# Kernel optimization log

Hardware: AMD Instinct MI355X
Metric: run time of the kernel (lower is better)

## Reference

```python
import jax, jax.numpy as jnp
import numpy as np

N_HEADS = 12
NEG_BIG = 1e10  # matches torch source's -10000000000.0 masking constant


def setup_inputs() -> dict:
    key = jax.random.key(0)
    ks = jax.random.split(key, 5)
    nb, ns, nf = 4, 2048, 768
    return {
        "x": jax.random.normal(ks[0], (nb, ns, nf), dtype=jnp.float32),
        "Wqkv_w": jax.random.normal(ks[1], (3 * nf, nf), dtype=jnp.float32) * 0.02,
        "Wqkv_b": jax.random.normal(ks[2], (3 * nf,), dtype=jnp.float32) * 0.02,
        "Wproj_w": jax.random.normal(ks[3], (nf, nf), dtype=jnp.float32) * 0.02,
        "Wproj_b": jax.random.normal(ks[4], (nf,), dtype=jnp.float32) * 0.02,
    }


def reference(x, Wqkv_w, Wqkv_b, Wproj_w, Wproj_b):
    nb, ns, nf = x.shape
    hd = nf // N_HEADS
    qkv = x @ Wqkv_w.T + Wqkv_b            # [b, s, 3f]
    q = qkv[..., :nf]                       # source bug: k and v are taken from q
    q = q.reshape(nb, ns, N_HEADS, hd).transpose(0, 2, 1, 3)  # [b, h, s, d]
    k = q
    v = q
    w = jnp.einsum("bhqd,bhkd->bhqk", q, k) * (1.0 / jnp.sqrt(jnp.float32(hd)))
    mask = jnp.tril(jnp.ones((ns, ns), dtype=x.dtype))
    w = jax.nn.softmax(w * mask - NEG_BIG * (1.0 - mask), axis=-1)
    a = jnp.einsum("bhqk,bhkd->bhqd", w, v)
    a = a.transpose(0, 2, 1, 3).reshape(nb, ns, nf)
    return a @ Wproj_w.T + Wproj_b
```

## Files before the change

### kernel.cpp

```cpp
#include <hip/hip_runtime.h>
#include <hip/hip_bf16.h>

#define NF 768
#define NHEADS 12
#define NSEQ 2048
#define NX (8192 * 768)
#define NW (768 * 768)

#define QSC 0.42466090f

typedef __attribute__((__ext_vector_type__(8))) __bf16 bfrag;
typedef __attribute__((__ext_vector_type__(4))) float f32x4;
typedef __attribute__((__ext_vector_type__(16))) float f32x16;

static __device__ __forceinline__ unsigned short bfu(float f) {
    union { __hip_bfloat16 h; unsigned short u; } v;
    v.h = __float2bfloat16(f);
    return v.u;
}

static __device__ __forceinline__ int packrn(float lo, float hi) {
    union { __hip_bfloat162 h; int i; } u;
    u.h.x = __float2bfloat16(lo);
    u.h.y = __float2bfloat16(hi);
    return u.i;
}

static __device__ __forceinline__ float exp2a(float x) {
#if __has_builtin(__builtin_amdgcn_exp2f)
    return __builtin_amdgcn_exp2f(x);
#else
    return exp2f(x);
#endif
}

static __device__ __forceinline__ void plswap(int& a, int& b, int hi) {
#if __has_builtin(__builtin_amdgcn_permlane32_swap)
    auto r = __builtin_amdgcn_permlane32_swap((unsigned)a, (unsigned)b, false, false);
    a = (int)r[0]; b = (int)r[1];
#else
    int ta = __shfl_xor(b, 32), tb = __shfl_xor(a, 32);
    a = hi ? ta : a;
    b = hi ? b : tb;
#endif
}

static __device__ __forceinline__ float xhalf(float v, int hi) {
#if __has_builtin(__builtin_amdgcn_permlane32_swap)
    union { float f; unsigned u; } c; c.f = v;
    auto r = __builtin_amdgcn_permlane32_swap(c.u, c.u, false, false);
    union { unsigned u; float f; } d; d.u = hi ? r[0] : r[1];
    return d.f;
#else
    return __shfl_xor(v, 32);
#endif
}

static __device__ __forceinline__ void gload16(const unsigned short* g, unsigned short* l) {
#if __has_builtin(__builtin_amdgcn_global_load_lds)
    __builtin_amdgcn_global_load_lds(
        (const __attribute__((address_space(1))) void*)g,
        (__attribute__((address_space(3))) void*)l, 16, 0, 0);
#else
    *(uint4*)l = *(const uint4*)g;
#endif
}

__global__ __launch_bounds__(256) void preconv(const float* __restrict__ x,
                                               const float* __restrict__ W1,
                                               const float* __restrict__ W2,
                                               unsigned short* __restrict__ xb,
                                               unsigned short* __restrict__ W1b,
                                               unsigned short* __restrict__ W2b) {
    const size_t i = ((size_t)blockIdx.x * 256 + threadIdx.x) * 8;
    const float* src;
    unsigned short* dst;
    float scl = 1.0f;
    if (i < (size_t)NX) {
        src = x + i; dst = xb + i;
    } else if (i < (size_t)NX + NW) {
        const size_t j = i - NX;
        src = W1 + j; dst = W1b + j; scl = QSC;
    } else {
        const size_t j = i - NX - NW;
        src = W2 + j; dst = W2b + j;
    }
    float4 v0 = *(const float4*)(src);
    float4 v1 = *(const float4*)(src + 4);
    uint4 o;
    o.x = (unsigned)packrn(v0.x * scl, v0.y * scl);
    o.y = (unsigned)packrn(v0.z * scl, v0.w * scl);
    o.z = (unsigned)packrn(v1.x * scl, v1.y * scl);
    o.w = (unsigned)packrn(v1.z * scl, v1.w * scl);
    *(uint4*)dst = o;
}

__global__ __launch_bounds__(256) void gemm_qkv(const unsigned short* __restrict__ A,
                                                const unsigned short* __restrict__ B,
                                                const float* __restrict__ bias,
                                                unsigned short* __restrict__ Qo) {
    __shared__ unsigned short As[64 * 32];
    __shared__ unsigned short Bs[128 * 32];
    const int t    = threadIdx.x;
    const int bm   = blockIdx.x / 6, bn = blockIdx.x % 6;
    const int m0   = bm * 64, n0 = bn * 128;
    const int lane = t & 63;
    const int wid  = t >> 6;
    const int wm   = (wid >> 1) * 32, wn = (wid & 1) * 64;

    const unsigned short* ga  = A + (size_t)(m0 + (t >> 2)) * NF + (t & 3) * 8;
    const unsigned short* gb  = B + (size_t)(n0 + (t >> 2)) * NF + (t & 3) * 8;
    const unsigned short* gb2 = gb + (size_t)64 * NF;

    f32x4 acc[2][4];
#pragma unroll
    for (int i = 0; i < 2; i++)
#pragma unroll
        for (int j = 0; j < 4; j++) acc[i][j] = (f32x4)0.0f;

    for (int k0 = 0; k0 < NF; k0 += 32) {
        gload16(ga + k0, &As[t * 8]);
        gload16(gb + k0, &Bs[t * 8]);
        gload16(gb2 + k0, &Bs[2048 + t * 8]);
        __syncthreads();

        bfrag af[2], bfr[4];
#pragma unroll
        for (int i = 0; i < 2; i++)
            af[i]  = *(const bfrag*)&As[(wm + i*16 + (lane & 15)) * 32 + (lane >> 4) * 8];
#pragma unroll
        for (int j = 0; j < 4; j++)
            bfr[j] = *(const bfrag*)&Bs[(wn + j*16 + (lane & 15)) * 32 + (lane >> 4) * 8];
#pragma unroll
        for (int i = 0; i < 2; i++)
#pragma unroll
            for (int j = 0; j < 4; j++)
                acc[i][j] = __builtin_amdgcn_mfma_f32_16x16x32_bf16(af[i], bfr[j], acc[i][j], 0, 0, 0);
        __syncthreads();
    }

#pragma unroll
    for (int j = 0; j < 4; j++) {
        const int col = n0 + wn + j*16 + (lane & 15);
        const float bq = QSC * bias[col];
#pragma unroll
        for (int i = 0; i < 2; i++) {
            const int rbase = m0 + wm + i*16 + ((lane >> 4) << 2);
#pragma unroll
            for (int r = 0; r < 4; r++)
                Qo[(size_t)(rbase + r) * NF + col] = bfu(acc[i][j][r] + bq);
        }
    }
}

__global__ __launch_bounds__(256) void gemm_proj(const unsigned short* __restrict__ A,
                                                 const unsigned short* __restrict__ B,
                                                 const float* __restrict__ bias,
                                                 float* __restrict__ out) {
    __shared__ unsigned short As[64 * 32];
    __shared__ unsigned short Bs[128 * 32];
    const int t    = threadIdx.x;
    const int bm   = blockIdx.x / 6, bn = blockIdx.x % 6;
    const int m0   = bm * 64, n0 = bn * 128;
    const int lane = t & 63;
    const int wid  = t >> 6;
    const int wm   = (wid >> 1) * 32, wn = (wid & 1) * 64;

    const unsigned short* ga  = A + (size_t)(m0 + (t >> 2)) * NF + (t & 3) * 8;
    const unsigned short* gb  = B + (size_t)(n0 + (t >> 2)) * NF + (t & 3) * 8;
    const unsigned short* gb2 = gb + (size_t)64 * NF;

    f32x4 acc[2][4];
#pragma unroll
    for (int i = 0; i < 2; i++)
#pragma unroll
        for (int j = 0; j < 4; j++) acc[i][j] = (f32x4)0.0f;

    for (int k0 = 0; k0 < NF; k0 += 32) {
        gload16(ga + k0, &As[t * 8]);
        gload16(gb + k0, &Bs[t * 8]);
        gload16(gb2 + k0, &Bs[2048 + t * 8]);
        __syncthreads();

        bfrag af[2], bfr[4];
#pragma unroll
        for (int i = 0; i < 2; i++)
            af[i]  = *(const bfrag*)&As[(wm + i*16 + (lane & 15)) * 32 + (lane >> 4) * 8];
#pragma unroll
        for (int j = 0; j < 4; j++)
            bfr[j] = *(const bfrag*)&Bs[(wn + j*16 + (lane & 15)) * 32 + (lane >> 4) * 8];
#pragma unroll
        for (int i = 0; i < 2; i++)
#pragma unroll
            for (int j = 0; j < 4; j++)
                acc[i][j] = __builtin_amdgcn_mfma_f32_16x16x32_bf16(af[i], bfr[j], acc[i][j], 0, 0, 0);
        __syncthreads();
    }

#pragma unroll
    for (int j = 0; j < 4; j++) {
        const int col = n0 + wn + j*16 + (lane & 15);
        const float bvv = bias[col];
#pragma unroll
        for (int i = 0; i < 2; i++) {
            const int rbase = m0 + wm + i*16 + ((lane >> 4) << 2);
#pragma unroll
            for (int r = 0; r < 4; r++)
                out[(size_t)(rbase + r) * NF + col] = acc[i][j][r] + bvv;
        }
    }
}

__global__ __launch_bounds__(128, 1) void attn(const unsigned short* __restrict__ Q,
                                               unsigned short* __restrict__ O) {
    const int pair = blockIdx.x;
    const int bh   = blockIdx.y;
    const int b    = bh / NHEADS, h = bh % NHEADS;
    const unsigned short* base = Q + (size_t)b * NSEQ * NF + h * 64;
    unsigned short*       ob   = O + (size_t)b * NSEQ * NF + h * 64;

    const int t   = threadIdx.x;
    const int w   = t >> 6;
    const int l31 = t & 31;
    const int hi  = (t >> 5) & 1;
    const int sw  = l31 & 7;
    const int svw = (l31 & 7) ^ ((l31 >> 2) & 7);

    __shared__ unsigned short Ks[64 * 64];
    __shared__ unsigned short Vt[64 * 64];

    for (int half = 0; half < 2; half++) {
        const int qt  = half ? (31 - pair) : pair;
        const int wq0 = qt * 64 + w * 32;
        const int qg  = wq0 + l31;

        bfrag qf[4];
#pragma unroll
        for (int c16 = 0; c16 < 4; c16++)
            qf[c16] = *(const bfrag*)(base + (size_t)qg * NF + c16*16 + hi*8);

        f32x16 o[2];
#pragma unroll
        for (int fd = 0; fd < 2; fd++)
#pragma unroll
            for (int r = 0; r < 16; r++) o[fd][r] = 0.0f;
        float m_ = -3.0e38f, l_ = 0.0f;

        const int ktend = qt + 1;
        for (int kt = 0; kt < ktend; kt++) {
            const int k0 = kt * 64;

            {
                const int r = t >> 1, c = t & 1;
                const unsigned short* kg = base + (size_t)(k0 + r) * NF + c * 32;
#pragma unroll
                for (int i = 0; i < 4; i++) {
                    uint4 v = *(const uint4*)(kg + i * 8);
                    const int u = (4 * c + i) ^ (r & 7);
                    *(uint4*)&Ks[r * 64 + u * 8] = v;
                }
            }
            {
                const int p = t & 15, g2 = t >> 4;
                const unsigned short* vg = base + (size_t)(k0 + 8 * g2) * NF + 4 * p;
                uint2 ld[8];
#pragma unroll
                for (int i = 0; i < 8; i++) ld[i] = *(const uint2*)(vg + (size_t)i * NF);
#pragma unroll
                for (int j = 0; j < 4; j++) {
                    const int d = 4 * p + j;
                    union { unsigned short h[8]; uint4 q; } wv;
#pragma unroll
                    for (int i = 0; i < 8; i++) wv.h[i] = ((const unsigned short*)&ld[i])[j];
                    const int u = g2 ^ (d & 7) ^ ((d >> 2) & 7);
                    *(uint4*)&Vt[d * 64 + u * 8] = wv.q;
                }
            }
            __syncthreads();

            const bool diag  = (kt == qt);
            const int  kb_hi = diag ? w : 1;

            f32x16 s[2];
            __builtin_amdgcn_s_setprio(1);
#pragma unroll
            for (int kblk = 0; kblk < 2; kblk++) {
                if (kblk <= kb_hi) {
                    f32x16 z;
#pragma unroll
                    for (int r = 0; r < 16; r++) z[r] = 0.0f;
#pragma unroll
                    for (int c16 = 0; c16 < 4; c16++) {
                        bfrag ka = *(const bfrag*)&Ks[(kblk*32 + l31)*64 + (((2*c16 + hi) ^ sw) * 8)];
                        z = __builtin_amdgcn_mfma_f32_32x32x16_bf16(ka, qf[c16], z, 0, 0, 0);
                    }
                    s[kblk] = z;
                }
            }
            __builtin_amdgcn_s_setprio(0);

            if (diag) {
                if (w == 0) {
#pragma unroll
                    for (int r = 0; r < 16; r++) {
                        const int kp = k0 + (r & 3) + 8*(r >> 2) + 4*hi;
                        if (kp > qg) s[0][r] = -1.0e30f;
                    }
                } else {
#pragma unroll
                    for (int r = 0; r < 16; r++) {
                        const int kp = k0 + 32 + (r & 3) + 8*(r >> 2) + 4*hi;
                        if (kp > qg) s[1][r] = -1.0e30f;
                    }
                }
            }

            float mx = -3.0e38f;
#pragma unroll
            for (int kblk = 0; kblk < 2; kblk++)
                if (kblk <= kb_hi) {
#pragma unroll
                    for (int r = 0; r < 16; r++) mx = fmaxf(mx, s[kblk][r]);
                }
            mx = fmaxf(mx, xhalf(mx, hi));

            const bool nogrow = __all(mx <= m_ + 8.0f);
            const float mn = nogrow ? m_ : fmaxf(m_, mx);
            float rs = 0.0f;
#pragma unroll
            for (int kblk = 0; kblk < 2; kblk++)
                if (kblk <= kb_hi) {
#pragma unroll
                    for (int r = 0; r < 16; r++) {
                        const float p = exp2a(s[kblk][r] - mn);
                        s[kblk][r] = p;
                        rs += p;
                    }
                }
            rs += xhalf(rs, hi);
            if (nogrow) {
                l_ += rs;
            } else {
                const float sc = exp2a(m_ - mn);
                l_ = l_ * sc + rs;
                m_ = mn;
#pragma unroll
                for (int fd = 0; fd < 2; fd++)
#pragma unroll
                    for (int r = 0; r < 16; r++) o[fd][r] *= sc;
            }

#pragma unroll
            for (int kblk = 0; kblk < 2; kblk++) {
                if (kblk <= kb_hi) {
                    int wv_[4][2];
#pragma unroll
                    for (int f = 0; f < 4; f++)
#pragma unroll
                        for (int rr = 0; rr < 2; rr++)
                            wv_[f][rr] = packrn(s[kblk][4*f + 2*rr], s[kblk][4*f + 2*rr + 1]);
#pragma unroll
                    for (int c = 0; c < 2; c++) {
                        int x0 = wv_[2*c][0], y0 = wv_[2*c+1][0];
                        plswap(x0, y0, hi);
                        int x1 = wv_[2*c][1], y1 = wv_[2*c+1][1];
                        plswap(x1, y1, hi);
                        union { int d[4]; bfrag f; } pf;
                        pf.d[0] = x0; pf.d[1] = x1; pf.d[2] = y0; pf.d[3] = y1;
                        const int ck = kblk*2 + c;
                        __builtin_amdgcn_s_setprio(1);
#pragma unroll
                        for (int fd = 0; fd < 2; fd++) {
                            bfrag va = *(const bfrag*)&Vt[(fd*32 + l31)*64 + (((2*ck + hi) ^ svw) * 8)];
                            o[fd] = __builtin_amdgcn_mfma_f32_32x32x16_bf16(va, pf.f, o[fd], 0, 0, 0);
                        }
                        __builtin_amdgcn_s_setprio(0);
                    }
                }
            }
            __syncthreads();
        }

        const float inv = 1.0f / (l_ * QSC);
#pragma unroll
        for (int fd = 0; fd < 2; fd++)
#pragma unroll
            for (int f = 0; f < 4; f++) {
                const int d0 = fd*32 + 8*f + 4*hi;
                uint2 pr;
                pr.x = (unsigned)packrn(o[fd][4*f+0]*inv, o[fd][4*f+1]*inv);
                pr.y = (unsigned)packrn(o[fd][4*f+2]*inv, o[fd][4*f+3]*inv);
                *(uint2*)(ob + (size_t)qg * NF + d0) = pr;
            }
    }
}

extern "C" void kernel_launch(void* const* d_in, const int* in_sizes, int n_in,
                              void* d_out, int out_size, void* d_ws, size_t ws_size,
                              hipStream_t stream) {
    const float* x    = (const float*)d_in[0];
    const float* Wqkv = (const float*)d_in[1];
    const float* bqkv = (const float*)d_in[2];
    const float* Wp   = (const float*)d_in[3];
    const float* bp   = (const float*)d_in[4];
    float* out        = (float*)d_out;

    unsigned short* Qws = (unsigned short*)d_ws;
    unsigned short* Aws = Qws + (size_t)NX;
    unsigned short* xb  = Aws + (size_t)NX;
    unsigned short* W1b = xb + (size_t)NX;
    unsigned short* W2b = W1b + (size_t)NW;

    preconv<<<3648, 256, 0, stream>>>(x, Wqkv, Wp, xb, W1b, W2b);
    gemm_qkv<<<768, 256, 0, stream>>>(xb, W1b, bqkv, Qws);
    attn<<<dim3(16, 48), 128, 0, stream>>>(Qws, Aws);
    gemm_proj<<<768, 256, 0, stream>>>(Aws, W2b, bp, out);
}
```

Before: 131.6 us.

## Double-buffer K/V tiles in attention with register prefetch of next tile

The attention kernel now keeps two LDS buffers for K and transposed V. It issues global loads for the next key tile into registers during the softmax and PV phase, then writes them to the alternate buffer before the barrier, leaving one sync per iteration. The aim is to hide global load latency behind MFMA work. In exchange it doubles LDS use and raises register pressure from the held prefetch values.

```diff
diff --git a/kernel.cpp b/kernel.cpp
--- a/kernel.cpp
+++ b/kernel.cpp
@@ -64,6 +64,34 @@
 #else
     *(uint4*)l = *(const uint4*)g;
 #endif
+}
+
+static __device__ __forceinline__ void loadt(const unsigned short* kgb, const unsigned short* vgb,
+                                             size_t off, uint4 (&kv)[4], uint2 (&vd)[8]) {
+#pragma unroll
+    for (int i = 0; i < 4; i++) kv[i] = *(const uint4*)(kgb + off + i * 8);
+#pragma unroll
+    for (int i = 0; i < 8; i++) vd[i] = *(const uint2*)(vgb + off + (size_t)i * NF);
+}
+
+static __device__ __forceinline__ void writet(int t, const uint4 (&kv)[4], const uint2 (&vd)[8],
+                                              unsigned short* Ksb, unsigned short* Vtb) {
+    const int kr = t >> 1, kc = t & 1;
+#pragma unroll
+    for (int i = 0; i < 4; i++) {
+        const int u = (4 * kc + i) ^ (kr & 7);
+        *(uint4*)&Ksb[kr * 64 + u * 8] = kv[i];
+    }
+    const int vp = t & 15, vg2 = t >> 4;
+#pragma unroll
+    for (int j = 0; j < 4; j++) {
+        const int d = 4 * vp + j;
+        union { unsigned short h[8]; uint4 q; } wv;
+#pragma unroll
+        for (int i = 0; i < 8; i++) wv.h[i] = ((const unsigned short*)&vd[i])[j];
+        const int u = vg2 ^ (d & 7) ^ ((d >> 2) & 7);
+        *(uint4*)&Vtb[d * 64 + u * 8] = wv.q;
+    }
 }
 
 __global__ __launch_bounds__(256) void preconv(const float* __restrict__ x,
@@ -226,8 +254,11 @@
     const int sw  = l31 & 7;
     const int svw = (l31 & 7) ^ ((l31 >> 2) & 7);
 
-    __shared__ unsigned short Ks[64 * 64];
-    __shared__ unsigned short Vt[64 * 64];
+    const unsigned short* kgb = base + (size_t)(t >> 1) * NF + (t & 1) * 32;
+    const unsigned short* vgb = base + (size_t)(8 * (t >> 4)) * NF + 4 * (t & 15);
+
+    __shared__ unsigned short Ks[2][64 * 64];
+    __shared__ unsigned short Vt[2][64 * 64];
 
     for (int half = 0; half < 2; half++) {
         const int qt  = half ? (31 - pair) : pair;
@@ -247,39 +278,20 @@
         float m_ = -3.0e38f, l_ = 0.0f;
 
         const int ktend = qt + 1;
+
+        uint4 kv[4];
+        uint2 vd[8];
+        loadt(kgb, vgb, 0, kv, vd);
+        writet(t, kv, vd, &Ks[0][0], &Vt[0][0]);
+        __syncthreads();
+
         for (int kt = 0; kt < ktend; kt++) {
+            const unsigned short* ksb = &Ks[kt & 1][0];
+            const unsigned short* vtb = &Vt[kt & 1][0];
             const int k0 = kt * 64;
-
-            {
-                const int r = t >> 1, c = t & 1;
-                const unsigned short* kg = base + (size_t)(k0 + r) * NF + c * 32;
-#pragma unroll
-                for (int i = 0; i < 4; i++) {
-                    uint4 v = *(const uint4*)(kg + i * 8);
-                    const int u = (4 * c + i) ^ (r & 7);
-                    *(uint4*)&Ks[r * 64 + u * 8] = v;
-                }
-            }
-            {
-                const int p = t & 15, g2 = t >> 4;
-                const unsigned short* vg = base + (size_t)(k0 + 8 * g2) * NF + 4 * p;
-                uint2 ld[8];
-#pragma unroll
-                for (int i = 0; i < 8; i++) ld[i] = *(const uint2*)(vg + (size_t)i * NF);
-#pragma unroll
-                for (int j = 0; j < 4; j++) {
-                    const int d = 4 * p + j;
-                    union { unsigned short h[8]; uint4 q; } wv;
-#pragma unroll
-                    for (int i = 0; i < 8; i++) wv.h[i] = ((const unsigned short*)&ld[i])[j];
-                    const int u = g2 ^ (d & 7) ^ ((d >> 2) & 7);
-                    *(uint4*)&Vt[d * 64 + u * 8] = wv.q;
-                }
-            }
-            __syncthreads();
-
             const bool diag  = (kt == qt);
             const int  kb_hi = diag ? w : 1;
+            const bool more  = (kt + 1 < ktend);
 
             f32x16 s[2];
             __builtin_amdgcn_s_setprio(1);
@@ -291,7 +303,7 @@
                     for (int r = 0; r < 16; r++) z[r] = 0.0f;
 #pragma unroll
                     for (int c16 = 0; c16 < 4; c16++) {
-                        bfrag ka = *(const bfrag*)&Ks[(kblk*32 + l31)*64 + (((2*c16 + hi) ^ sw) * 8)];
+                        bfrag ka = *(const bfrag*)&ksb[(kblk*32 + l31)*64 + (((2*c16 + hi) ^ sw) * 8)];
                         z = __builtin_amdgcn_mfma_f32_32x32x16_bf16(ka, qf[c16], z, 0, 0, 0);
                     }
                     s[kblk] = z;
@@ -350,6 +362,8 @@
                     for (int r = 0; r < 16; r++) o[fd][r] *= sc;
             }
 
+            if (more) loadt(kgb, vgb, (size_t)(kt + 1) * 64 * NF, kv, vd);
+
 #pragma unroll
             for (int kblk = 0; kblk < 2; kblk++) {
                 if (kblk <= kb_hi) {
@@ -371,13 +385,15 @@
                         __builtin_amdgcn_s_setprio(1);
 #pragma unroll
                         for (int fd = 0; fd < 2; fd++) {
-                            bfrag va = *(const bfrag*)&Vt[(fd*32 + l31)*64 + (((2*ck + hi) ^ svw) * 8)];
+                            bfrag va = *(const bfrag*)&vtb[(fd*32 + l31)*64 + (((2*ck + hi) ^ svw) * 8)];
                             o[fd] = __builtin_amdgcn_mfma_f32_32x32x16_bf16(va, pf.f, o[fd], 0, 0, 0);
                         }
                         __builtin_amdgcn_s_setprio(0);
                     }
                 }
             }
+
+            if (more) writet(t, kv, vd, &Ks[(kt + 1) & 1][0], &Vt[(kt + 1) & 1][0]);
             __syncthreads();
         }
 
```

Measured after the change: 190.8 us. 45.0% more time.

## Use 128-query tiles with 4 waves per attention block, drop pair balancing

Applied to the files above, without the earlier changes.

Each attention block now has 256 threads (4 waves) covering a 128-row query tile, replacing the two-wave block that handled a balanced pair of 64-row tiles in sequence. Blocks are issued longest-first (qt = 15 - blockIdx.x) so the causal imbalance is left to the hardware scheduler instead of the explicit pairing. K tile loading and V transpose loading now run on separate thread halves, and waves whose queries lie entirely before a key tile skip its compute. This shares each K/V tile across more waves, but blocks are now uneven in length, and some waves sit idle on tiles near the diagonal.

```diff
diff --git a/kernel.cpp b/kernel.cpp
--- a/kernel.cpp
+++ b/kernel.cpp
@@ -211,11 +211,11 @@
     }
 }
 
-__global__ __launch_bounds__(128, 1) void attn(const unsigned short* __restrict__ Q,
+__global__ __launch_bounds__(256, 1) void attn(const unsigned short* __restrict__ Q,
                                                unsigned short* __restrict__ O) {
-    const int pair = blockIdx.x;
-    const int bh   = blockIdx.y;
-    const int b    = bh / NHEADS, h = bh % NHEADS;
+    const int qt = 15 - blockIdx.x;
+    const int bh = blockIdx.y;
+    const int b  = bh / NHEADS, h = bh % NHEADS;
     const unsigned short* base = Q + (size_t)b * NSEQ * NF + h * 64;
     unsigned short*       ob   = O + (size_t)b * NSEQ * NF + h * 64;
 
@@ -229,57 +229,56 @@
     __shared__ unsigned short Ks[64 * 64];
     __shared__ unsigned short Vt[64 * 64];
 
-    for (int half = 0; half < 2; half++) {
-        const int qt  = half ? (31 - pair) : pair;
-        const int wq0 = qt * 64 + w * 32;
-        const int qg  = wq0 + l31;
-
-        bfrag qf[4];
-#pragma unroll
-        for (int c16 = 0; c16 < 4; c16++)
-            qf[c16] = *(const bfrag*)(base + (size_t)qg * NF + c16*16 + hi*8);
-
-        f32x16 o[2];
-#pragma unroll
-        for (int fd = 0; fd < 2; fd++)
-#pragma unroll
-            for (int r = 0; r < 16; r++) o[fd][r] = 0.0f;
-        float m_ = -3.0e38f, l_ = 0.0f;
-
-        const int ktend = qt + 1;
-        for (int kt = 0; kt < ktend; kt++) {
-            const int k0 = kt * 64;
-
-            {
-                const int r = t >> 1, c = t & 1;
-                const unsigned short* kg = base + (size_t)(k0 + r) * NF + c * 32;
-#pragma unroll
-                for (int i = 0; i < 4; i++) {
-                    uint4 v = *(const uint4*)(kg + i * 8);
-                    const int u = (4 * c + i) ^ (r & 7);
-                    *(uint4*)&Ks[r * 64 + u * 8] = v;
-                }
-            }
-            {
-                const int p = t & 15, g2 = t >> 4;
-                const unsigned short* vg = base + (size_t)(k0 + 8 * g2) * NF + 4 * p;
-                uint2 ld[8];
-#pragma unroll
-                for (int i = 0; i < 8; i++) ld[i] = *(const uint2*)(vg + (size_t)i * NF);
-#pragma unroll
-                for (int j = 0; j < 4; j++) {
-                    const int d = 4 * p + j;
-                    union { unsigned short h[8]; uint4 q; } wv;
-#pragma unroll
-                    for (int i = 0; i < 8; i++) wv.h[i] = ((const unsigned short*)&ld[i])[j];
-                    const int u = g2 ^ (d & 7) ^ ((d >> 2) & 7);
-                    *(uint4*)&Vt[d * 64 + u * 8] = wv.q;
-                }
-            }
-            __syncthreads();
-
-            const bool diag  = (kt == qt);
-            const int  kb_hi = diag ? w : 1;
+    const int wq0 = qt * 128 + w * 32;
+    const int qg  = wq0 + l31;
+
+    bfrag qf[4];
+#pragma unroll
+    for (int c16 = 0; c16 < 4; c16++)
+        qf[c16] = *(const bfrag*)(base + (size_t)qg * NF + c16*16 + hi*8);
+
+    f32x16 o[2];
+#pragma unroll
+    for (int fd = 0; fd < 2; fd++)
+#pragma unroll
+        for (int r = 0; r < 16; r++) o[fd][r] = 0.0f;
+    float m_ = -3.0e38f, l_ = 0.0f;
+
+    const int ktend = 2 * qt + 2;
+    for (int kt = 0; kt < ktend; kt++) {
+        const int k0 = kt * 64;
+
+        if (t < 128) {
+            const int r = t >> 1, c = t & 1;
+            const unsigned short* kg = base + (size_t)(k0 + r) * NF + c * 32;
+#pragma unroll
+            for (int i = 0; i < 4; i++) {
+                uint4 v = *(const uint4*)(kg + i * 8);
+                const int u = (4 * c + i) ^ (r & 7);
+                *(uint4*)&Ks[r * 64 + u * 8] = v;
+            }
+        } else {
+            const int tt = t - 128;
+            const int p = tt & 15, g2 = tt >> 4;
+            const unsigned short* vg = base + (size_t)(k0 + 8 * g2) * NF + 4 * p;
+            uint2 ld[8];
+#pragma unroll
+            for (int i = 0; i < 8; i++) ld[i] = *(const uint2*)(vg + (size_t)i * NF);
+#pragma unroll
+            for (int j = 0; j < 4; j++) {
+                const int d = 4 * p + j;
+                union { unsigned short hh[8]; uint4 q; } wv;
+#pragma unroll
+                for (int i = 0; i < 8; i++) wv.hh[i] = ((const unsigned short*)&ld[i])[j];
+                const int u = g2 ^ (d & 7) ^ ((d >> 2) & 7);
+                *(uint4*)&Vt[d * 64 + u * 8] = wv.q;
+            }
+        }
+        __syncthreads();
+
+        const int rel = wq0 + 31 - k0;
+        if (rel >= 0) {
+            const int kb_hi = min(rel >> 5, 1);
 
             f32x16 s[2];
             __builtin_amdgcn_s_setprio(1);
@@ -299,18 +298,13 @@
             }
             __builtin_amdgcn_s_setprio(0);
 
-            if (diag) {
-                if (w == 0) {
+#pragma unroll
+            for (int kblk = 0; kblk < 2; kblk++) {
+                if (kblk <= kb_hi && (k0 + kblk*32 + 31 > wq0)) {
 #pragma unroll
                     for (int r = 0; r < 16; r++) {
-                        const int kp = k0 + (r & 3) + 8*(r >> 2) + 4*hi;
-                        if (kp > qg) s[0][r] = -1.0e30f;
-                    }
-                } else {
-#pragma unroll
-                    for (int r = 0; r < 16; r++) {
-                        const int kp = k0 + 32 + (r & 3) + 8*(r >> 2) + 4*hi;
-                        if (kp > qg) s[1][r] = -1.0e30f;
+                        const int kp = k0 + kblk*32 + (r & 3) + 8*(r >> 2) + 4*hi;
+                        if (kp > qg) s[kblk][r] = -1.0e30f;
                     }
                 }
             }
@@ -378,21 +372,21 @@
                     }
                 }
             }
-            __syncthreads();
         }
-
-        const float inv = 1.0f / (l_ * QSC);
-#pragma unroll
-        for (int fd = 0; fd < 2; fd++)
-#pragma unroll
-            for (int f = 0; f < 4; f++) {
-                const int d0 = fd*32 + 8*f + 4*hi;
-                uint2 pr;
-                pr.x = (unsigned)packrn(o[fd][4*f+0]*inv, o[fd][4*f+1]*inv);
-                pr.y = (unsigned)packrn(o[fd][4*f+2]*inv, o[fd][4*f+3]*inv);
-                *(uint2*)(ob + (size_t)qg * NF + d0) = pr;
-            }
-    }
+        __syncthreads();
+    }
+
+    const float inv = 1.0f / (l_ * QSC);
+#pragma unroll
+    for (int fd = 0; fd < 2; fd++)
+#pragma unroll
+        for (int f = 0; f < 4; f++) {
+            const int d0 = fd*32 + 8*f + 4*hi;
+            uint2 pr;
+            pr.x = (unsigned)packrn(o[fd][4*f+0]*inv, o[fd][4*f+1]*inv);
+            pr.y = (unsigned)packrn(o[fd][4*f+2]*inv, o[fd][4*f+3]*inv);
+            *(uint2*)(ob + (size_t)qg * NF + d0) = pr;
+        }
 }
 
 extern "C" void kernel_launch(void* const* d_in, const int* in_sizes, int n_in,
@@ -413,6 +407,6 @@
 
     preconv<<<3648, 256, 0, stream>>>(x, Wqkv, Wp, xb, W1b, W2b);
     gemm_qkv<<<768, 256, 0, stream>>>(xb, W1b, bqkv, Qws);
-    attn<<<dim3(16, 48), 128, 0, stream>>>(Qws, Aws);
+    attn<<<dim3(16, 48), 256, 0, stream>>>(Qws, Aws);
     gemm_proj<<<768, 256, 0, stream>>>(Aws, W2b, bp, out);
 }
```

Result: slower. 149.1 us (+13.3%).
